# Kernel optimization log

Hardware: AMD Instinct MI355X
Metric: run time of the kernel (lower is better)

Reference implementation:

```python
import jax, jax.numpy as jnp
import numpy as np

N_SEQ, N_RES, C_M = 512, 256, 256
C_OUTER, C_Z = 32, 128
LN_EPS = 1e-5
NORM_EPS = 1e-3


def setup_inputs() -> dict:
    key = jax.random.key(0)
    ks = jax.random.split(key, 6)
    f32 = jnp.float32
    return {
        "act": jax.random.normal(ks[0], (N_SEQ, N_RES, C_M), f32),
        "mask": jnp.ones((N_SEQ, N_RES), f32),
        # LayerNorm params (create_scale=True, create_offset=True)
        "ln_scale": jnp.ones((C_M,), f32),
        "ln_offset": jnp.zeros((C_M,), f32),
        # left/right projections, 'linear' (VarianceScaling fan_in scale=1)
        "left_w": (jax.random.normal(ks[1], (C_M, C_OUTER), f32) / np.float32(np.sqrt(C_M))),
        "left_b": jnp.zeros((C_OUTER,), f32),
        "right_w": (jax.random.normal(ks[2], (C_M, C_OUTER), f32) / np.float32(np.sqrt(C_M))),
        "right_b": jnp.zeros((C_OUTER,), f32),
        # output_w: VarianceScaling(scale=2.0, fan_in) over (c_outer, c_outer) input dims
        "output_w": (jax.random.normal(ks[3], (C_OUTER, C_OUTER, C_Z), f32)
                     * np.float32(np.sqrt(2.0 / (C_OUTER * C_OUTER)))),
        "output_b": jnp.zeros((C_Z,), f32),
    }


def reference(act, mask, ln_scale, ln_offset, left_w, left_b, right_w, right_b,
              output_w, output_b):
    # LayerNorm over last axis
    mu = jnp.mean(act, axis=-1, keepdims=True)
    var = jnp.var(act, axis=-1, keepdims=True)
    x = (act - mu) * jax.lax.rsqrt(var + LN_EPS) * ln_scale + ln_offset

    m = mask[..., None]  # [N_seq, N_res, 1]
    left = m * (jnp.einsum('abm,mc->abc', x, left_w) + left_b)    # [A,B,Co]
    right = m * (jnp.einsum('abm,me->abe', x, right_w) + right_b)  # [A,D,Co]

    # mean outer product: sum over MSA depth a -> [B, D, Co, Co]
    op = jnp.einsum('abc,ade->bdce', left, right)
    out = jnp.einsum('bdce,cef->bdf', op, output_w) + output_b  # [B, D, Cz]

    # normalization by pairwise mask counts
    norm = jnp.einsum('ab,ad->bd', mask, mask)[..., None]  # [B, D, 1]
    return out / (NORM_EPS + norm)
```

## Files before the change

### kernel.cpp

```cpp
#include <hip/hip_runtime.h>
#include <hip/hip_bf16.h>
#include <stdint.h>

typedef short bf16x8 __attribute__((ext_vector_type(8)));
typedef float f32x4 __attribute__((ext_vector_type(4)));
typedef unsigned short u16x4 __attribute__((ext_vector_type(4)));
typedef unsigned short u16x8 __attribute__((ext_vector_type(8)));

#define GLOAD16(g, l) __builtin_amdgcn_global_load_lds( \
    (const __attribute__((address_space(1))) void*)(g), \
    (__attribute__((address_space(3))) void*)(l), 16, 0, 0)

__device__ __forceinline__ unsigned short f2bf(float f) {
  unsigned u = __float_as_uint(f);
  unsigned r = (u + 0x7fffu + ((u >> 16) & 1u)) >> 16;
  return (unsigned short)r;
}

__global__ __launch_bounds__(256) void prep_norm_k(
    const float* __restrict__ lw, const float* __restrict__ rw,
    const float* __restrict__ ow, const float* __restrict__ mask,
    unsigned short* __restrict__ Wt, unsigned short* __restrict__ wfragG,
    float* __restrict__ nrm) {
  const int bid = blockIdx.x;
  if (bid < 512) {
    int idx = bid * 256 + threadIdx.x;
    if (idx < 131072) {
      int f = idx >> 10, k2 = idx & 1023;
      int e = k2 >> 5, c = k2 & 31;
      Wt[idx] = f2bf(ow[(size_t)((c << 5) + e) * 128 + f]);
    }
    if (idx < 16384) {
      int frag = idx >> 9, lane = (idx >> 3) & 63, j = idx & 7;
      int wc = frag >> 4, ni = (frag >> 3) & 1, kk = frag & 7;
      int mrow = lane & 15, g = lane >> 4;
      int c = wc * 32 + ni * 16 + mrow;
      int k = kk * 32 + g * 8 + j;
      wfragG[idx] = f2bf(c < 32 ? lw[k * 32 + c] : rw[k * 32 + (c - 32)]);
    }
  } else {
    const int b = bid - 512, d = threadIdx.x;
    float s = 0.f;
    #pragma unroll 8
    for (int a = 0; a < 512; ++a)
      s += mask[a * 256 + b] * mask[a * 256 + d];
    nrm[(b << 8) + d] = s;
  }
}

__global__ __launch_bounds__(256, 4) void ln_proj(
    const float* __restrict__ act, const float* __restrict__ mask,
    const float* __restrict__ lns, const float* __restrict__ lno,
    const float* __restrict__ lb, const float* __restrict__ rb,
    const unsigned short* __restrict__ wfragG,
    unsigned short* __restrict__ Lt, unsigned short* __restrict__ Rt) {
  __shared__ char smem[32768];
  const int tid = threadIdx.x;
  const int lane = tid & 63;
  const int w = tid >> 6;
  const int b = blockIdx.y;
  const int a0 = blockIdx.x << 6;
  const int l = tid & 15;
  const int rg = tid >> 4;

  f32x4 sc[4], of[4];
  #pragma unroll
  for (int j = 0; j < 4; ++j) {
    sc[j] = *(const f32x4*)(lns + (l << 4) + (j << 2));
    of[j] = *(const f32x4*)(lno + (l << 4) + (j << 2));
  }

  #pragma unroll
  for (int i = 0; i < 4; ++i) {
    const int r = rg + (i << 4);
    const float* src = act + ((size_t)(a0 + r) * 256 + b) * 256 + (l << 4);
    f32x4 xv[4];
    #pragma unroll
    for (int j = 0; j < 4; ++j) xv[j] = *(const f32x4*)(src + (j << 2));
    float s = 0.f, sq = 0.f;
    #pragma unroll
    for (int j = 0; j < 4; ++j) {
      f32x4 v = xv[j];
      s += v[0] + v[1] + v[2] + v[3];
      sq += v[0] * v[0] + v[1] * v[1] + v[2] * v[2] + v[3] * v[3];
    }
    s += __shfl_xor(s, 1); sq += __shfl_xor(sq, 1);
    s += __shfl_xor(s, 2); sq += __shfl_xor(sq, 2);
    s += __shfl_xor(s, 4); sq += __shfl_xor(sq, 4);
    s += __shfl_xor(s, 8); sq += __shfl_xor(sq, 8);
    const float mu = s * (1.f / 256.f);
    const float rs = rsqrtf(sq * (1.f / 256.f) - mu * mu + 1e-5f);
    #pragma unroll
    for (int hh = 0; hh < 2; ++hh) {
      u16x8 pk;
      #pragma unroll
      for (int j2 = 0; j2 < 2; ++j2) {
        const int j = (hh << 1) + j2;
        #pragma unroll
        for (int e = 0; e < 4; ++e)
          pk[(j2 << 2) + e] = f2bf((xv[j][e] - mu) * rs * sc[j][e] + of[j][e]);
      }
      const int c = (l << 1) + hh;
      *(u16x8*)(smem + (r << 9) + ((c ^ (r & 7)) << 4)) = pk;
    }
  }
  __syncthreads();

  const int wr = w >> 1, wc = w & 1;
  const int mrow = lane & 15, g = lane >> 4;
  f32x4 acc[2][2];
  #pragma unroll
  for (int i = 0; i < 2; ++i)
    #pragma unroll
    for (int jj = 0; jj < 2; ++jj) acc[i][jj] = (f32x4){0.f, 0.f, 0.f, 0.f};
  #pragma unroll
  for (int kk = 0; kk < 8; ++kk) {
    bf16x8 af[2], bfr[2];
    #pragma unroll
    for (int mi = 0; mi < 2; ++mi) {
      const int row = (wr << 5) + (mi << 4) + mrow;
      af[mi] = *(const bf16x8*)(smem + (row << 9) + ((((kk << 2) + g) ^ (row & 7)) << 4));
    }
    #pragma unroll
    for (int ni = 0; ni < 2; ++ni)
      bfr[ni] = *(const bf16x8*)(wfragG + (size_t)((((wc << 1) + ni) << 3) + kk) * 512 + (lane << 3));
    #pragma unroll
    for (int mi = 0; mi < 2; ++mi)
      #pragma unroll
      for (int ni = 0; ni < 2; ++ni)
        acc[mi][ni] = __builtin_amdgcn_mfma_f32_16x16x32_bf16(af[mi], bfr[ni], acc[mi][ni], 0, 0, 0);
  }
  __syncthreads();

  #pragma unroll
  for (int ni = 0; ni < 2; ++ni) {
    const int c = (wc << 5) + (ni << 4) + mrow;
    const float bias = (wc == 0) ? lb[(ni << 4) + mrow] : rb[(ni << 4) + mrow];
    #pragma unroll
    for (int mi = 0; mi < 2; ++mi) {
      const int aB = (wr << 5) + (mi << 4) + (g << 2);
      u16x4 pk;
      #pragma unroll
      for (int qq = 0; qq < 4; ++qq) {
        const float mk = mask[(size_t)(a0 + aB + qq) * 256 + b];
        pk[qq] = f2bf((acc[mi][ni][qq] + bias) * mk);
      }
      *(u16x4*)(smem + (c << 7) + ((((aB >> 3) & 7) ^ (c & 7)) << 4) + ((aB & 7) << 1)) = pk;
    }
  }
  __syncthreads();

  #pragma unroll
  for (int s = 0; s < 2; ++s) {
    const int c = (w << 4) + (s << 3) + (lane >> 3);
    const int gr = lane & 7;
    const u16x8 v = *(const u16x8*)(smem + (c << 7) + ((gr ^ (c & 7)) << 4));
    unsigned short* dst = (c < 32) ? Lt : Rt;
    *(u16x8*)(dst + (size_t)(b * 32 + (c & 31)) * 512 + a0 + (gr << 3)) = v;
  }
}

__global__ __launch_bounds__(512, 2) void gemm_fused(
    const unsigned short* __restrict__ Lt, const unsigned short* __restrict__ Rt,
    const unsigned short* __restrict__ Wt, const float* __restrict__ nrm,
    const float* __restrict__ outb, float* __restrict__ out) {
  __shared__ char smem[131072];
  const int tid = threadIdx.x;
  const int lane = tid & 63;
  const int w = tid >> 6;
  const int wr = w >> 2, wc = w & 3;
  const int mrow = lane & 15, g = lane >> 4;

  const int bid = blockIdx.x;
  const int xcd = bid & 7, jj_ = bid >> 3;
  const int mb = ((jj_ >> 5) << 3) | (jj_ & 7);
  const int nb = (xcd << 2) | ((jj_ >> 3) & 3);
  const int m0i = mb << 8, n0i = nb << 8;

  const int scol = (((tid & 7) ^ ((tid >> 3) & 7)) << 3);

  f32x4 acc[8][4];
  #pragma unroll
  for (int i = 0; i < 8; ++i)
    #pragma unroll
    for (int jj = 0; jj < 4; ++jj) acc[i][jj] = (f32x4){0.f, 0.f, 0.f, 0.f};

  auto STG = [&](const unsigned short* gsrc, int baserow, int dstoff, int kt) {
    GLOAD16(gsrc + ((size_t)(baserow + (tid >> 3)) << 9) + (kt << 6) + scol,
            smem + dstoff + (tid << 4));
  };

  STG(Rt, n0i, 32768, 0);        STG(Rt, n0i + 64, 40960, 0);
  STG(Rt, n0i + 128, 49152, 0);  STG(Rt, n0i + 192, 57344, 0);
  STG(Lt, m0i, 0, 0);            STG(Lt, m0i + 128, 16384, 0);
  STG(Lt, m0i + 64, 8192, 0);    STG(Lt, m0i + 192, 24576, 0);
  asm volatile("s_waitcnt vmcnt(2)" ::: "memory");
  __builtin_amdgcn_s_barrier();

  #pragma unroll 1
  for (int t = 0; t < 8; ++t) {
    const int cbuf = (t & 1) << 16;
    const int nbuf = ((t + 1) & 1) << 16;
    const int k1 = t + 1;
    const bool pfe = (t < 7);
    bf16x8 bfr[4][2];
    #pragma unroll
    for (int p = 0; p < 4; ++p) {
      const int h = p >> 1, kk = p & 1;
      bf16x8 af[4];
      #pragma unroll
      for (int mi_ = 0; mi_ < 4; ++mi_) {
        af[mi_] = *(const bf16x8*)(smem + cbuf + (((wr << 1) + h) << 13) +
                                   (((mi_ << 4) + mrow) << 7) +
                                   ((((kk << 2) + g) ^ (mrow & 7)) << 4));
      }
      if (p < 2) {
        #pragma unroll
        for (int ni = 0; ni < 4; ++ni)
          bfr[ni][p] = *(const bf16x8*)(smem + cbuf + 32768 + (wc << 13) +
                                        (((ni << 4) + mrow) << 7) +
                                        ((((p << 2) + g) ^ (mrow & 7)) << 4));
      }
      if (pfe) {
        if (p == 0)      { STG(Rt, n0i, nbuf + 32768, k1);       STG(Rt, n0i + 64, nbuf + 40960, k1); }
        else if (p == 1) { STG(Rt, n0i + 128, nbuf + 49152, k1); STG(Rt, n0i + 192, nbuf + 57344, k1); }
        else if (p == 2) { STG(Lt, m0i, nbuf, k1);               STG(Lt, m0i + 128, nbuf + 16384, k1); }
        else             { STG(Lt, m0i + 64, nbuf + 8192, k1);   STG(Lt, m0i + 192, nbuf + 24576, k1); }
      }
      asm volatile("s_waitcnt lgkmcnt(0)" ::: "memory");
      __builtin_amdgcn_sched_barrier(0);
      __builtin_amdgcn_s_setprio(1);
      #pragma unroll
      for (int mi_ = 0; mi_ < 4; ++mi_)
        #pragma unroll
        for (int ni = 0; ni < 4; ++ni)
          acc[(h << 2) + mi_][ni] = __builtin_amdgcn_mfma_f32_16x16x32_bf16(
              af[mi_], bfr[ni][kk], acc[(h << 2) + mi_][ni], 0, 0, 0);
      __builtin_amdgcn_s_setprio(0);
      if (p == 1) {
        if (t < 7) asm volatile("s_waitcnt vmcnt(4)" ::: "memory");
        else       asm volatile("s_waitcnt vmcnt(0)" ::: "memory");
      } else if (p == 3 && pfe) {
        asm volatile("s_waitcnt vmcnt(2)" ::: "memory");
      }
      __builtin_amdgcn_s_barrier();
    }
  }

  #pragma unroll
  for (int mi = 0; mi < 8; ++mi) {
    #pragma unroll
    for (int ni = 0; ni < 4; ++ni) {
      const int p = (((wr << 2) + (mi >> 1)) << 3) | ((wc << 1) + (ni >> 1));
      const int ow_ = ((ni & 1) << 10) + (mrow << 6) + ((mi & 1) << 5) + (g << 3);
      u16x4 pk;
      #pragma unroll
      for (int qq = 0; qq < 4; ++qq) pk[qq] = f2bf(acc[mi][ni][qq]);
      *(u16x4*)(smem + (p << 11) + (ow_ ^ ((p & 7) << 4) ^ (((ow_ >> 7) & 7) << 4))) = pk;
    }
  }
  __syncthreads();

  f32x4 invn[4];
  #pragma unroll
  for (int pg = 0; pg < 4; ++pg) {
    const int bb = (mb << 3) + (pg << 1) + (g >> 1);
    const f32x4 nv = *(const f32x4*)(nrm + (bb << 8) + (nb << 3) + ((g & 1) << 2));
    #pragma unroll
    for (int qq = 0; qq < 4; ++qq) invn[pg][qq] = __builtin_amdgcn_rcpf(1e-3f + nv[qq]);
  }

  const int f0 = w << 4;
  f32x4 acc2[4];
  #pragma unroll
  for (int i = 0; i < 4; ++i) acc2[i] = (f32x4){0.f, 0.f, 0.f, 0.f};
  const unsigned short* wrow = Wt + (size_t)(f0 + mrow) * 1024;
  #pragma unroll 8
  for (int kk2 = 0; kk2 < 32; ++kk2) {
    const bf16x8 b2 = *(const bf16x8*)(wrow + (kk2 << 5) + (g << 3));
    const int orr = (kk2 << 6) + (g << 4);
    #pragma unroll
    for (int pg = 0; pg < 4; ++pg) {
      const int prow = (pg << 4) + mrow;
      const bf16x8 a2 = *(const bf16x8*)(smem + (prow << 11) +
          (orr ^ ((prow & 7) << 4) ^ (((orr >> 7) & 7) << 4)));
      acc2[pg] = __builtin_amdgcn_mfma_f32_16x16x32_bf16(a2, b2, acc2[pg], 0, 0, 0);
    }
  }

  const float ob_ = outb[f0 + mrow];
  #pragma unroll
  for (int pg = 0; pg < 4; ++pg) {
    #pragma unroll
    for (int qq = 0; qq < 4; ++qq) {
      const int p = (pg << 4) + (g << 2) + qq;
      const int bb = (mb << 3) + (p >> 3);
      const int dd = (nb << 3) + (p & 7);
      out[(size_t)((bb << 8) + dd) * 128 + f0 + mrow] = (acc2[pg][qq] + ob_) * invn[pg][qq];
    }
  }
}

extern "C" void kernel_launch(void* const* d_in, const int* in_sizes, int n_in,
                              void* d_out, int out_size, void* d_ws, size_t ws_size,
                              hipStream_t stream) {
  const float* act = (const float*)d_in[0];
  const float* mask = (const float*)d_in[1];
  const float* lns = (const float*)d_in[2];
  const float* lno = (const float*)d_in[3];
  const float* lw = (const float*)d_in[4];
  const float* lb = (const float*)d_in[5];
  const float* rw = (const float*)d_in[6];
  const float* rbv = (const float*)d_in[7];
  const float* ow = (const float*)d_in[8];
  const float* ob = (const float*)d_in[9];
  float* out = (float*)d_out;
  char* ws = (char*)d_ws;

  unsigned short* Lt = (unsigned short*)(ws);
  unsigned short* Rt = (unsigned short*)(ws + 8388608);
  unsigned short* Wt = (unsigned short*)(ws + 16777216);
  unsigned short* wfragG = (unsigned short*)(ws + 17039360);
  float* nrm = (float*)(ws + 17072128);

  hipLaunchKernelGGL(prep_norm_k, dim3(768), dim3(256), 0, stream,
                     lw, rw, ow, mask, Wt, wfragG, nrm);
  hipLaunchKernelGGL(ln_proj, dim3(8, 256), dim3(256), 0, stream,
                     act, mask, lns, lno, lb, rbv, wfragG, Lt, Rt);
  hipLaunchKernelGGL(gemm_fused, dim3(1024), dim3(512), 0, stream,
                     Lt, Rt, Wt, nrm, ob, out);
}
```

Baseline: 153.6 us.

## Load B fragments from global into registers instead of staging through LDS

The right-operand tiles are now read by each wave straight from global memory into registers, prefetched one k-step ahead, instead of being staged through shared memory. The k-step loop is restructured from four phases into two halves, each issuing both k sub-slices of MFMAs, with retuned vmcnt waits. The aim is to cut LDS traffic and shared-memory reads for B. In exchange, B global loads are duplicated across waves, register pressure rises, and the hand-counted waitcnt sequencing gets more fragile.

```diff
diff --git a/kernel.cpp b/kernel.cpp
--- a/kernel.cpp
+++ b/kernel.cpp
@@ -185,67 +185,80 @@
     #pragma unroll
     for (int jj = 0; jj < 4; ++jj) acc[i][jj] = (f32x4){0.f, 0.f, 0.f, 0.f};
 
-  auto STG = [&](const unsigned short* gsrc, int baserow, int dstoff, int kt) {
-    GLOAD16(gsrc + ((size_t)(baserow + (tid >> 3)) << 9) + (kt << 6) + scol,
-            smem + dstoff + (tid << 4));
+  auto STGA = [&](int buf, int c, int kt) {
+    GLOAD16(Lt + ((size_t)(m0i + (c << 6) + (tid >> 3)) << 9) + (kt << 6) + scol,
+            smem + buf + (c << 13) + (tid << 4));
   };
-
-  STG(Rt, n0i, 32768, 0);        STG(Rt, n0i + 64, 40960, 0);
-  STG(Rt, n0i + 128, 49152, 0);  STG(Rt, n0i + 192, 57344, 0);
-  STG(Lt, m0i, 0, 0);            STG(Lt, m0i + 128, 16384, 0);
-  STG(Lt, m0i + 64, 8192, 0);    STG(Lt, m0i + 192, 24576, 0);
-  asm volatile("s_waitcnt vmcnt(2)" ::: "memory");
+  const unsigned short* Bbase = Rt + ((size_t)(n0i + (wc << 6) + mrow) << 9) + (g << 3);
+  auto BLD = [&](int ni, int kk, int kt) {
+    return *(const bf16x8*)(Bbase + (size_t)(ni << 13) + (kt << 6) + (kk << 5));
+  };
+
+  STGA(0, 0, 0); STGA(0, 2, 0); STGA(0, 1, 0); STGA(0, 3, 0);
+  bf16x8 bk0[4], bk1[4], bkn0[4], bkn1[4];
+  #pragma unroll
+  for (int ni = 0; ni < 4; ++ni) { bk0[ni] = BLD(ni, 0, 0); bk1[ni] = BLD(ni, 1, 0); }
+  asm volatile("s_waitcnt vmcnt(0)" ::: "memory");
   __builtin_amdgcn_s_barrier();
 
   #pragma unroll 1
   for (int t = 0; t < 8; ++t) {
     const int cbuf = (t & 1) << 16;
     const int nbuf = ((t + 1) & 1) << 16;
-    const int k1 = t + 1;
     const bool pfe = (t < 7);
-    bf16x8 bfr[4][2];
-    #pragma unroll
-    for (int p = 0; p < 4; ++p) {
-      const int h = p >> 1, kk = p & 1;
-      bf16x8 af[4];
-      #pragma unroll
-      for (int mi_ = 0; mi_ < 4; ++mi_) {
-        af[mi_] = *(const bf16x8*)(smem + cbuf + (((wr << 1) + h) << 13) +
-                                   (((mi_ << 4) + mrow) << 7) +
-                                   ((((kk << 2) + g) ^ (mrow & 7)) << 4));
-      }
-      if (p < 2) {
+    #pragma unroll
+    for (int h = 0; h < 2; ++h) {
+      bf16x8 af[2][4];
+      #pragma unroll
+      for (int kk = 0; kk < 2; ++kk)
         #pragma unroll
-        for (int ni = 0; ni < 4; ++ni)
-          bfr[ni][p] = *(const bf16x8*)(smem + cbuf + 32768 + (wc << 13) +
-                                        (((ni << 4) + mrow) << 7) +
-                                        ((((p << 2) + g) ^ (mrow & 7)) << 4));
-      }
+        for (int mi = 0; mi < 4; ++mi) {
+          af[kk][mi] = *(const bf16x8*)(smem + cbuf + (((wr << 1) + h) << 13) +
+                                        (((mi << 4) + mrow) << 7) +
+                                        ((((kk << 2) + g) ^ (mrow & 7)) << 4));
+        }
       if (pfe) {
-        if (p == 0)      { STG(Rt, n0i, nbuf + 32768, k1);       STG(Rt, n0i + 64, nbuf + 40960, k1); }
-        else if (p == 1) { STG(Rt, n0i + 128, nbuf + 49152, k1); STG(Rt, n0i + 192, nbuf + 57344, k1); }
-        else if (p == 2) { STG(Lt, m0i, nbuf, k1);               STG(Lt, m0i + 128, nbuf + 16384, k1); }
-        else             { STG(Lt, m0i + 64, nbuf + 8192, k1);   STG(Lt, m0i + 192, nbuf + 24576, k1); }
+        if (h == 0) {
+          STGA(nbuf, 0, t + 1); STGA(nbuf, 2, t + 1);
+        } else {
+          STGA(nbuf, 1, t + 1);
+          #pragma unroll
+          for (int ni = 0; ni < 4; ++ni) bkn0[ni] = BLD(ni, 0, t + 1);
+          STGA(nbuf, 3, t + 1);
+          #pragma unroll
+          for (int ni = 0; ni < 4; ++ni) bkn1[ni] = BLD(ni, 1, t + 1);
+        }
       }
       asm volatile("s_waitcnt lgkmcnt(0)" ::: "memory");
       __builtin_amdgcn_sched_barrier(0);
       __builtin_amdgcn_s_setprio(1);
       #pragma unroll
-      for (int mi_ = 0; mi_ < 4; ++mi_)
+      for (int mi = 0; mi < 4; ++mi)
         #pragma unroll
         for (int ni = 0; ni < 4; ++ni)
-          acc[(h << 2) + mi_][ni] = __builtin_amdgcn_mfma_f32_16x16x32_bf16(
-              af[mi_], bfr[ni][kk], acc[(h << 2) + mi_][ni], 0, 0, 0);
+          acc[(h << 2) + mi][ni] = __builtin_amdgcn_mfma_f32_16x16x32_bf16(
+              af[0][mi], bk0[ni], acc[(h << 2) + mi][ni], 0, 0, 0);
+      #pragma unroll
+      for (int mi = 0; mi < 4; ++mi)
+        #pragma unroll
+        for (int ni = 0; ni < 4; ++ni)
+          acc[(h << 2) + mi][ni] = __builtin_amdgcn_mfma_f32_16x16x32_bf16(
+              af[1][mi], bk1[ni], acc[(h << 2) + mi][ni], 0, 0, 0);
       __builtin_amdgcn_s_setprio(0);
-      if (p == 1) {
-        if (t < 7) asm volatile("s_waitcnt vmcnt(4)" ::: "memory");
-        else       asm volatile("s_waitcnt vmcnt(0)" ::: "memory");
-      } else if (p == 3 && pfe) {
-        asm volatile("s_waitcnt vmcnt(2)" ::: "memory");
+      if (h == 0) {
+        if (t < 7) asm volatile("s_waitcnt vmcnt(6)" ::: "memory");
+        else       asm volatile("s_waitcnt vmcnt(4)" ::: "memory");
+      } else {
+        if (t < 7) asm volatile("s_waitcnt vmcnt(10)" ::: "memory");
       }
       __builtin_amdgcn_s_barrier();
     }
-  }
+    if (pfe) {
+      #pragma unroll
+      for (int ni = 0; ni < 4; ++ni) { bk0[ni] = bkn0[ni]; bk1[ni] = bkn1[ni]; }
+    }
+  }
+  __syncthreads();
 
   #pragma unroll
   for (int mi = 0; mi < 8; ++mi) {
```

Measured after the change: 190.5 us. 24.0% more time.
